# Optimization experiments

Measured on AMD Instinct MI355X. Metric: run time of the kernel, lower is better.

The kernel has to match this reference:

```python
import jax, jax.numpy as jnp
import numpy as np

S, B, F, H = 1024, 512, 128, 3

def setup_inputs() -> dict:
    key = jax.random.key(0)
    ks = jax.random.split(key, 7)
    x = jax.random.normal(ks[0], (S, B, F), dtype=jnp.float32)
    # Gumbel(0,1) noise = -log(-log(U))
    u = jax.random.uniform(ks[1], (S, B, H), dtype=jnp.float32, minval=1e-6, maxval=1.0 - 1e-6)
    gumbel = -jnp.log(-jnp.log(u))
    bound = 1.0 / np.sqrt(H)  # torch nn.RNN default init U(-1/sqrt(H), 1/sqrt(H))
    W_ih = jax.random.uniform(ks[2], (H, F), dtype=jnp.float32, minval=-bound, maxval=bound)
    W_hh = jax.random.uniform(ks[3], (H, H), dtype=jnp.float32, minval=-bound, maxval=bound)
    b_ih = jax.random.uniform(ks[4], (H,), dtype=jnp.float32, minval=-bound, maxval=bound)
    b_hh = jax.random.uniform(ks[5], (H,), dtype=jnp.float32, minval=-bound, maxval=bound)
    signal = jnp.array([[-1.0], [0.0], [1.0]], dtype=jnp.float32)
    return {"x": x, "gumbel": gumbel, "W_ih": W_ih, "W_hh": W_hh,
            "b_ih": b_ih, "b_hh": b_hh, "signal": signal}

def reference(x, gumbel, W_ih, W_hh, b_ih, b_hh, signal):
    # Precompute the input projection for all timesteps (one big GEMM).
    xp = jnp.einsum('sbf,hf->sbh', x, W_ih) + b_ih  # (S, B, H)

    def step(h, xt):
        h = jnp.tanh(xt + h @ W_hh.T + b_hh)  # (B, H)
        return h, h

    h0 = jnp.zeros((x.shape[1], W_hh.shape[0]), dtype=x.dtype)
    hT, output = jax.lax.scan(step, h0, xp)  # output: (S, B, H)

    # gumbel_softmax(hard=True), tau=1
    logits = output + gumbel
    y_soft = jax.nn.softmax(logits, axis=-1)
    idx = jnp.argmax(logits, axis=-1)
    y_hard = jax.nn.one_hot(idx, logits.shape[-1], dtype=y_soft.dtype)
    y = y_hard + y_soft - jax.lax.stop_gradient(y_soft)

    delta = y @ signal            # (S, B, 1)
    hidden_state = hT[None]       # (1, B, H) matching torch RNN hidden output
    return delta, hidden_state
```

## Files before the change

### kernel.cpp

```cpp
#include <hip/hip_runtime.h>
#include <hip/hip_bf16.h>


#define S_DIM 1024
#define B_DIM 512
#define F_DIM 128

__global__ __launch_bounds__(256) void k_inproj(
    const float* __restrict__ x,
    const float* __restrict__ gumbel,
    const float* __restrict__ W,
    const float* __restrict__ b_ih,
    const float* __restrict__ b_hh,
    float* __restrict__ xpk)
{
    int tid = blockIdx.x * 256 + threadIdx.x;
    int row = tid >> 5;
    int l   = tid & 31;

    float4 w0 = ((const float4*)(W))[l];
    float4 w1 = ((const float4*)(W + F_DIM))[l];
    float4 w2 = ((const float4*)(W + 2 * F_DIM))[l];

    float4 v = ((const float4*)x)[(size_t)row * 32 + l];

    float p0 = v.x * w0.x + v.y * w0.y + v.z * w0.z + v.w * w0.w;
    float p1 = v.x * w1.x + v.y * w1.y + v.z * w1.z + v.w * w1.w;
    float p2 = v.x * w2.x + v.y * w2.y + v.z * w2.z + v.w * w2.w;

#pragma unroll
    for (int m = 1; m <= 16; m <<= 1) {
        p0 += __shfl_xor(p0, m, 64);
        p1 += __shfl_xor(p1, m, 64);
        p2 += __shfl_xor(p2, m, 64);
    }

    if (l < 3) {
        float a = (l == 0) ? p0 : ((l == 1) ? p1 : p2);
        xpk[(size_t)row * 8 + l] = a + b_ih[l] + b_hh[l];
    } else if (l >= 4 && l < 7) {
        xpk[(size_t)row * 8 + l] = gumbel[(size_t)row * 3 + (l - 4)];
    }
}

__device__ __forceinline__ float tanh_fast(float xv) {
    float e = __expf(2.0f * xv);
    return 1.0f - 2.0f * __builtin_amdgcn_rcpf(e + 1.0f);
}

#define U_PF 16

__global__ __launch_bounds__(64) void k_scan(
    const float* __restrict__ xpk,
    const float* __restrict__ W_hh,
    const float* __restrict__ signal,
    float* __restrict__ out)
{
    int b = blockIdx.x * 64 + threadIdx.x;

    float w00 = W_hh[0], w01 = W_hh[1], w02 = W_hh[2];
    float w10 = W_hh[3], w11 = W_hh[4], w12 = W_hh[5];
    float w20 = W_hh[6], w21 = W_hh[7], w22 = W_hh[8];
    float s0v = signal[0], s1v = signal[1], s2v = signal[2];

    float h0 = 0.f, h1 = 0.f, h2 = 0.f;

    const float4* xg = (const float4*)xpk;

    float4 bufx[U_PF], bufg[U_PF];
#pragma unroll
    for (int i = 0; i < U_PF; ++i) {
        size_t r = (size_t)i * B_DIM + b;
        bufx[i] = xg[2 * r];
        bufg[i] = xg[2 * r + 1];
    }

#define STEP(sidx, xv, gv)                                                  \
    {                                                                       \
        float a0 = xv.x + w00 * h0 + w01 * h1 + w02 * h2;                   \
        float a1 = xv.y + w10 * h0 + w11 * h1 + w12 * h2;                   \
        float a2 = xv.z + w20 * h0 + w21 * h1 + w22 * h2;                   \
        h0 = tanh_fast(a0);                                                 \
        h1 = tanh_fast(a1);                                                 \
        h2 = tanh_fast(a2);                                                 \
        float l0 = h0 + gv.x, l1 = h1 + gv.y, l2 = h2 + gv.z;               \
        float d = (l2 > l0 && l2 > l1) ? s2v : ((l1 > l0) ? s1v : s0v);     \
        out[(sidx) * B_DIM + b] = d;                                        \
    }

    for (int s0 = 0; s0 < S_DIM - U_PF; s0 += U_PF) {
#pragma unroll
        for (int i = 0; i < U_PF; ++i) {
            float4 xv = bufx[i];
            float4 gv = bufg[i];
            size_t r = (size_t)(s0 + i + U_PF) * B_DIM + b;
            bufx[i] = xg[2 * r];
            bufg[i] = xg[2 * r + 1];
            STEP(s0 + i, xv, gv)
        }
    }
#pragma unroll
    for (int i = 0; i < U_PF; ++i) {
        float4 xv = bufx[i];
        float4 gv = bufg[i];
        STEP(S_DIM - U_PF + i, xv, gv)
    }
#undef STEP

    float* hid = out + (size_t)S_DIM * B_DIM + (size_t)b * 3;
    hid[0] = h0; hid[1] = h1; hid[2] = h2;
}

extern "C" void kernel_launch(void* const* d_in, const int* in_sizes, int n_in,
                              void* d_out, int out_size, void* d_ws, size_t ws_size,
                              hipStream_t stream) {
    const float* x      = (const float*)d_in[0];
    const float* gumbel = (const float*)d_in[1];
    const float* W_ih   = (const float*)d_in[2];
    const float* W_hh   = (const float*)d_in[3];
    const float* b_ih   = (const float*)d_in[4];
    const float* b_hh   = (const float*)d_in[5];
    const float* signal = (const float*)d_in[6];

    float* xpk = (float*)d_ws;
    float* out = (float*)d_out;

    k_inproj<<<(S_DIM * B_DIM * 32) / 256, 256, 0, stream>>>(
        x, gumbel, W_ih, b_ih, b_hh, xpk);
    k_scan<<<B_DIM / 64, 64, 0, stream>>>(xpk, W_hh, signal, out);
}
```

Baseline: 480.5 us.

## Stream scan inputs through triple-buffered LDS via async global_load_lds

Replaces the per-thread register prefetch ring in the recurrent scan with a triple-buffered LDS pipeline. Tiles of 8 timesteps are loaded with direct global-to-LDS loads, synchronised by hand-written vmcnt waits, and read back through swizzled LDS offsets. The goal is to keep more memory requests in flight for the latency-bound serial scan while freeing registers. In exchange it depends on hard-coded waitcnt encodings and swizzle layout, and it adds LDS reads to the critical path.

```diff
diff --git a/kernel.cpp b/kernel.cpp
--- a/kernel.cpp
+++ b/kernel.cpp
@@ -5,6 +5,8 @@
 #define S_DIM 1024
 #define B_DIM 512
 #define F_DIM 128
+#define TILE_S 8
+#define NT (S_DIM / TILE_S)
 
 __global__ __launch_bounds__(256) void k_inproj(
     const float* __restrict__ x,
@@ -48,7 +50,12 @@
     return 1.0f - 2.0f * __builtin_amdgcn_rcpf(e + 1.0f);
 }
 
-#define U_PF 16
+#define WAITCNT_VM16 0x4F70
+#define WAITCNT_VM24 0x4F78
+#define WAITCNT_VM8  0x0F78
+
+typedef __attribute__((address_space(1))) const void gas_void;
+typedef __attribute__((address_space(3))) void las_void;
 
 __global__ __launch_bounds__(64) void k_scan(
     const float* __restrict__ xpk,
@@ -56,7 +63,18 @@
     const float* __restrict__ signal,
     float* __restrict__ out)
 {
-    int b = blockIdx.x * 64 + threadIdx.x;
+    __shared__ float lds[3 * TILE_S * 512];
+
+    int tid = threadIdx.x;
+    int b0  = blockIdx.x * 64;
+    int b   = b0 + tid;
+
+    int hsw   = (tid & 1) ^ ((tid >> 3) & 1);
+    int goffA = ((tid >> 1) * 32) + (hsw << 4);
+    int goffB = ((32 + (tid >> 1)) * 32) + (hsw << 4);
+    int x   = (tid >> 2) & 1;
+    int rdx = tid * 8 + (x << 2);
+    int rdg = tid * 8 + ((x ^ 1) << 2);
 
     float w00 = W_hh[0], w01 = W_hh[1], w02 = W_hh[2];
     float w10 = W_hh[3], w11 = W_hh[4], w12 = W_hh[5];
@@ -65,47 +83,51 @@
 
     float h0 = 0.f, h1 = 0.f, h2 = 0.f;
 
-    const float4* xg = (const float4*)xpk;
+    const char* xpc = (const char*)xpk;
 
-    float4 bufx[U_PF], bufg[U_PF];
+    auto issue_tile = [&](int t, int buf) {
+        const char* gtile = xpc + (((size_t)t * TILE_S * B_DIM) + b0) * 32;
+        float* lb = &lds[buf * (TILE_S * 512)];
 #pragma unroll
-    for (int i = 0; i < U_PF; ++i) {
-        size_t r = (size_t)i * B_DIM + b;
-        bufx[i] = xg[2 * r];
-        bufg[i] = xg[2 * r + 1];
+        for (int i = 0; i < TILE_S; ++i) {
+            const char* gs = gtile + (size_t)i * (B_DIM * 32);
+            __builtin_amdgcn_global_load_lds(
+                (gas_void*)(gs + goffA), (las_void*)(lb + i * 512),       16, 0, 0);
+            __builtin_amdgcn_global_load_lds(
+                (gas_void*)(gs + goffB), (las_void*)(lb + i * 512 + 256), 16, 0, 0);
+        }
+    };
+
+    issue_tile(0, 0);
+    issue_tile(1, 1);
+
+    int bufc = 0;
+    for (int t = 0; t < NT; ++t) {
+        if (t == 0)           __builtin_amdgcn_s_waitcnt(WAITCNT_VM16);
+        else if (t == NT - 1) __builtin_amdgcn_s_waitcnt(WAITCNT_VM8);
+        else                  __builtin_amdgcn_s_waitcnt(WAITCNT_VM24);
+        __builtin_amdgcn_sched_barrier(0);
+
+        const float* lb = &lds[bufc * (TILE_S * 512)];
+#pragma unroll
+        for (int i = 0; i < TILE_S; ++i) {
+            float4 xv = *(const float4*)(lb + i * 512 + rdx);
+            float4 gv = *(const float4*)(lb + i * 512 + rdg);
+            float a0 = xv.x + w00 * h0 + w01 * h1 + w02 * h2;
+            float a1 = xv.y + w10 * h0 + w11 * h1 + w12 * h2;
+            float a2 = xv.z + w20 * h0 + w21 * h1 + w22 * h2;
+            h0 = tanh_fast(a0);
+            h1 = tanh_fast(a1);
+            h2 = tanh_fast(a2);
+            float l0 = h0 + gv.x, l1 = h1 + gv.y, l2 = h2 + gv.z;
+            float d = (l2 > l0 && l2 > l1) ? s2v : ((l1 > l0) ? s1v : s0v);
+            out[(t * TILE_S + i) * B_DIM + b] = d;
+        }
+        __builtin_amdgcn_sched_barrier(0);
+
+        if (t + 2 < NT) issue_tile(t + 2, (t + 2) % 3);
+        bufc = (bufc == 2) ? 0 : bufc + 1;
     }
-
-#define STEP(sidx, xv, gv)                                                  \
-    {                                                                       \
-        float a0 = xv.x + w00 * h0 + w01 * h1 + w02 * h2;                   \
-        float a1 = xv.y + w10 * h0 + w11 * h1 + w12 * h2;                   \
-        float a2 = xv.z + w20 * h0 + w21 * h1 + w22 * h2;                   \
-        h0 = tanh_fast(a0);                                                 \
-        h1 = tanh_fast(a1);                                                 \
-        h2 = tanh_fast(a2);                                                 \
-        float l0 = h0 + gv.x, l1 = h1 + gv.y, l2 = h2 + gv.z;               \
-        float d = (l2 > l0 && l2 > l1) ? s2v : ((l1 > l0) ? s1v : s0v);     \
-        out[(sidx) * B_DIM + b] = d;                                        \
-    }
-
-    for (int s0 = 0; s0 < S_DIM - U_PF; s0 += U_PF) {
-#pragma unroll
-        for (int i = 0; i < U_PF; ++i) {
-            float4 xv = bufx[i];
-            float4 gv = bufg[i];
-            size_t r = (size_t)(s0 + i + U_PF) * B_DIM + b;
-            bufx[i] = xg[2 * r];
-            bufg[i] = xg[2 * r + 1];
-            STEP(s0 + i, xv, gv)
-        }
-    }
-#pragma unroll
-    for (int i = 0; i < U_PF; ++i) {
-        float4 xv = bufx[i];
-        float4 gv = bufg[i];
-        STEP(S_DIM - U_PF + i, xv, gv)
-    }
-#undef STEP
 
     float* hid = out + (size_t)S_DIM * B_DIM + (size_t)b * 3;
     hid[0] = h0; hid[1] = h1; hid[2] = h2;
```

Result: slower. 528.4 us (+10.0%).
